# Optimization experiments

Measured on AMD Instinct MI355X. Metric: run time of the kernel, lower is better.

The kernel has to match this reference:

```python
import jax, jax.numpy as jnp
import numpy as np

H = W = 2048


def _grad(x, kernel):
    # torch F.conv2d(x, kernel, stride=1, padding=1); kernel [2,1,2,1] (OIHW)
    # output: [N, 2, H+1, W+2]
    y = jax.lax.conv_general_dilated(
        x, kernel, window_strides=(1, 1), padding=[(1, 1), (1, 1)],
        dimension_numbers=("NCHW", "OIHW", "NCHW"))
    return jnp.abs(y)


def _grayscale(r3):
    # emulates to_pil_image (mul 255 -> uint8) + PIL 'L' conversion + to_tensor (/255)
    # PIL: L = (R*19595 + G*38470 + B*7471 + 0x8000) >> 16
    q = jnp.floor(jnp.clip(r3, 0.0, 1.0) * 255.0)
    gs = jnp.floor((q[0] * 19595.0 + q[1] * 38470.0 + q[2] * 7471.0 + 32768.0) / 65536.0) / 255.0
    # PIL round-trip breaks autograd in the original -> detached here too
    return jax.lax.stop_gradient(gs)[None, None]  # [1,1,H,W]


def _histeq(im, nbins=256):
    # numpy: histogram(density=True) -> cumsum -> /cdf[-1] -> interp(x, bins[:-1], cdf)
    flat = im.reshape(-1)
    hist, edges = jnp.histogram(flat, bins=nbins, density=True)
    cdf = jnp.cumsum(hist)
    cdf = cdf / cdf[-1]
    return jnp.interp(flat, edges[:-1], cdf).reshape(im.shape)


def setup_inputs() -> dict:
    key = jax.random.key(0)
    k1, k2, k3 = jax.random.split(key, 3)
    return {
        "input_im": jax.random.uniform(k1, (1, 3, H, W), dtype=jnp.float32),
        "R": jax.random.uniform(k2, (1, 3, H, W), dtype=jnp.float32),
        "L": jax.random.uniform(k3, (1, 1, H, W), dtype=jnp.float32),
    }


def reference(input_im, R, L):
    kx = jnp.array([0.0, 0.0, -1.0, 1.0], dtype=jnp.float32).reshape(2, 1, 2, 1)
    ky = jnp.transpose(kx, (2, 1, 0, 3))  # torch permute(2,1,0,3)

    # histogram-equalized target (detached in original via .detach().cpu().numpy())
    im_max = jnp.max(input_im, axis=1, keepdims=True)           # [1,1,H,W]
    im_eq = jax.lax.stop_gradient(_histeq(im_max[0]))[None]     # [1,1,H,W]

    # recon_loss_low
    L3 = jnp.concatenate([L, L, L], axis=1)
    recon_low = jnp.mean(jnp.abs(R * L3 - input_im))

    # recon_loss_low_eq
    R_max = jnp.max(R, axis=1, keepdims=True)
    recon_low_eq = jnp.mean(jnp.abs(R_max - im_eq))

    # R_low_loss_smooth (grayscale is detached)
    Rg = _grayscale(R[0])                  # [1,1,H,W]
    a = _grad(Rg, kx)                      # [1,2,H+1,W+2]
    b = _grad(Rg, ky)
    r_smooth = jnp.mean(a + b)             # torch.abs of already-abs values

    # Ismooth_loss_low: smooth(L, R)
    ismooth = jnp.mean(_grad(L, kx) * jnp.exp(-10.0 * a)
                       + _grad(L, ky) * jnp.exp(-10.0 * b))

    return recon_low + 0.1 * ismooth + 0.1 * recon_low_eq + 0.01 * r_smooth
```

## Files before the change

### kernel.cpp

```cpp
#include <hip/hip_runtime.h>
#include <stdint.h>

#define HH 2048
#define WW 2048
#define HW (HH * WW)
#define N4 (HW / 4)
#define FB 512
#define G1H 256
#define G3M 512
#define STRIDE (G1H * 1024)


__device__ __forceinline__ float gray_pil(float r, float g, float b) {
    float qr = floorf(fminf(fmaxf(r, 0.f), 1.f) * 255.f);
    float qg = floorf(fminf(fmaxf(g, 0.f), 1.f) * 255.f);
    float qb = floorf(fminf(fmaxf(b, 0.f), 1.f) * 255.f);
    float s = floorf((qr * 19595.f + qg * 38470.f + qb * 7471.f + 32768.f) * (1.f / 65536.f));
    return s * (1.f / 255.f);
}

__global__ __launch_bounds__(1024, 1)
void hist_k(const float* __restrict__ im, uint32_t* __restrict__ ctl) {
    __shared__ uint32_t lh[FB];
    __shared__ uint32_t sc[256];
    __shared__ uint32_t smm[2];
    __shared__ uint32_t lastf;
    int t = threadIdx.x;
    if (t < FB) lh[t] = 0u;
    __syncthreads();

    const float4* im4 = (const float4*)im;
    int tid = blockIdx.x * 1024 + t;
    float4 A0 = im4[tid],              B0 = im4[tid + N4],              C0 = im4[tid + 2 * N4];
    float4 A1 = im4[tid + STRIDE],     B1 = im4[tid + STRIDE + N4],     C1 = im4[tid + STRIDE + 2 * N4];
    float4 A2 = im4[tid + 2 * STRIDE], B2 = im4[tid + 2 * STRIDE + N4], C2 = im4[tid + 2 * STRIDE + 2 * N4];
    float4 A3 = im4[tid + 3 * STRIDE], B3 = im4[tid + 3 * STRIDE + N4], C3 = im4[tid + 3 * STRIDE + 2 * N4];

#define HBIN(a, b, c) { \
        float m0 = fmaxf(a.x, fmaxf(b.x, c.x)); \
        float m1 = fmaxf(a.y, fmaxf(b.y, c.y)); \
        float m2 = fmaxf(a.z, fmaxf(b.z, c.z)); \
        float m3 = fmaxf(a.w, fmaxf(b.w, c.w)); \
        int b0 = (int)(m0 * (float)FB); b0 = b0 < 0 ? 0 : (b0 > FB - 1 ? FB - 1 : b0); \
        int b1 = (int)(m1 * (float)FB); b1 = b1 < 0 ? 0 : (b1 > FB - 1 ? FB - 1 : b1); \
        int b2 = (int)(m2 * (float)FB); b2 = b2 < 0 ? 0 : (b2 > FB - 1 ? FB - 1 : b2); \
        int b3 = (int)(m3 * (float)FB); b3 = b3 < 0 ? 0 : (b3 > FB - 1 ? FB - 1 : b3); \
        atomicAdd(&lh[b0], 1u); atomicAdd(&lh[b1], 1u); \
        atomicAdd(&lh[b2], 1u); atomicAdd(&lh[b3], 1u); }
    HBIN(A0, B0, C0)
    HBIN(A1, B1, C1)
    HBIN(A2, B2, C2)
    HBIN(A3, B3, C3)
#undef HBIN

    __syncthreads();
    if (t < 256) {
        int pr = (t + blockIdx.x * 7) & 255;
        unsigned long long v = (unsigned long long)lh[2 * pr]
                             | ((unsigned long long)lh[2 * pr + 1] << 32);
        if (v) atomicAdd((unsigned long long*)&ctl[2 * pr], v);
    }
    __syncthreads();
    if (t == 0) {
        __threadfence();
        lastf = (atomicAdd(&ctl[518], 1u) == G1H - 1) ? 1u : 0u;
    }
    __syncthreads();
    if (!lastf) return;

    if (t < FB) lh[t] = atomicAdd(&ctl[t], 0u);
    if (t < 256) sc[t] = 0u;
    if (t == 0) { smm[0] = FB; smm[1] = 0u; }
    __syncthreads();
    if (t < FB && lh[t]) { atomicMin(&smm[0], (uint32_t)t); atomicMax(&smm[1], (uint32_t)t); }
    __syncthreads();
    float gmin = (float)smm[0] * (1.0f / (float)FB);
    float gmax = (float)(smm[1] + 1u) * (1.0f / (float)FB);
    float inv_dw = 256.0f / (gmax - gmin);
    if (t < FB && lh[t]) {
        float c = ((float)t + 0.5f) * (1.0f / (float)FB);
        int q = (int)((c - gmin) * inv_dw);
        q = q < 0 ? 0 : (q > 255 ? 255 : q);
        atomicAdd(&sc[q], lh[t]);
    }
    __syncthreads();
    for (int d = 1; d < 256; d <<= 1) {
        uint32_t v = (t < 256 && t >= d) ? sc[t - d] : 0u;
        __syncthreads();
        if (t < 256) sc[t] += v;
        __syncthreads();
    }
    float* cf = (float*)ctl;
    if (t < 256) cf[t] = (float)((double)sc[t] * (1.0 / (double)HW));
    if (t == 0) { cf[256] = gmin; cf[257] = gmax; }
}

__device__ __forceinline__ void px(float r0, float r1, float r2,
                                   float i0, float i1, float i2, float l,
                                   float& rgp, float& lp,
                                   const float* __restrict__ scdf, float gmin, float inv_dw,
                                   float& a0, float& a1, float& a2,
                                   float& a3, float& a4, float& a5) {
    a0 += fabsf(r0 * l - i0) + fabsf(r1 * l - i1) + fabsf(r2 * l - i2);
    float rmax = fmaxf(r0, fmaxf(r1, r2));
    float imax = fmaxf(i0, fmaxf(i1, i2));
    float t = (imax - gmin) * inv_dw;
    t = fmaxf(t, 0.f);
    int bi = (int)t;
    float eq;
    if (bi >= 255) eq = scdf[255];
    else {
        float fr = t - (float)bi;
        eq = scdf[bi] + fr * (scdf[bi + 1] - scdf[bi]);
    }
    a1 += fabsf(rmax - eq);
    float rg = gray_pil(r0, r1, r2);
    a3 += rg;
    a5 += l * __expf(-10.f * rg);
    float drg = fabsf(rg - rgp);
    a2 += drg;
    a4 += fabsf(l - lp) * __expf(-10.f * drg);
    rgp = rg;
    lp = l;
}

__global__ __launch_bounds__(1024, 1)
void main_k(const float* __restrict__ im, const float* __restrict__ R,
            const float* __restrict__ L, uint32_t* __restrict__ ctl,
            float* __restrict__ part, int use_part,
            float* __restrict__ out) {
    __shared__ float scdf[256];
    __shared__ float red[6][16];
    __shared__ uint32_t lastf;
    int t = threadIdx.x;

    const float* cf = (const float*)ctl;
    if (t < 256) scdf[t] = cf[t];
    float gmin = cf[256];
    float gmax = cf[257];
    float inv_dw = 256.0f / (gmax - gmin);
    __syncthreads();

    int w = (t & 511) * 4;
    int h0 = blockIdx.x * 4 + ((t >> 9) * 2);
    const int p1 = h0 * WW + w;
    const int p2 = p1 + WW;

    float4 Pa, Pb, Pc, Pl;
    if (h0 > 0) {
        int pp = p1 - WW;
        Pa = *(const float4*)(R + pp);
        Pb = *(const float4*)(R + pp + HW);
        Pc = *(const float4*)(R + pp + 2 * HW);
        Pl = *(const float4*)(L + pp);
    }
    float4 r0a = *(const float4*)(R + p1);
    float4 r0b = *(const float4*)(R + p1 + HW);
    float4 r0c = *(const float4*)(R + p1 + 2 * HW);
    float4 i0a = *(const float4*)(im + p1);
    float4 i0b = *(const float4*)(im + p1 + HW);
    float4 i0c = *(const float4*)(im + p1 + 2 * HW);
    float4 l0  = *(const float4*)(L + p1);
    float4 r1a = *(const float4*)(R + p2);
    float4 r1b = *(const float4*)(R + p2 + HW);
    float4 r1c = *(const float4*)(R + p2 + 2 * HW);
    float4 i1a = *(const float4*)(im + p2);
    float4 i1b = *(const float4*)(im + p2 + HW);
    float4 i1c = *(const float4*)(im + p2 + 2 * HW);
    float4 l1  = *(const float4*)(L + p2);

    float a0 = 0.f, a1 = 0.f, a2 = 0.f, a3 = 0.f, a4 = 0.f, a5 = 0.f;
    float rgp[4], lp[4];
    if (h0 > 0) {
        rgp[0] = gray_pil(Pa.x, Pb.x, Pc.x); lp[0] = Pl.x;
        rgp[1] = gray_pil(Pa.y, Pb.y, Pc.y); lp[1] = Pl.y;
        rgp[2] = gray_pil(Pa.z, Pb.z, Pc.z); lp[2] = Pl.z;
        rgp[3] = gray_pil(Pa.w, Pb.w, Pc.w); lp[3] = Pl.w;
    } else {
        rgp[0] = rgp[1] = rgp[2] = rgp[3] = 0.f;
        lp[0] = lp[1] = lp[2] = lp[3] = 0.f;
    }

    px(r0a.x, r0b.x, r0c.x, i0a.x, i0b.x, i0c.x, l0.x, rgp[0], lp[0], scdf, gmin, inv_dw, a0, a1, a2, a3, a4, a5);
    px(r0a.y, r0b.y, r0c.y, i0a.y, i0b.y, i0c.y, l0.y, rgp[1], lp[1], scdf, gmin, inv_dw, a0, a1, a2, a3, a4, a5);
    px(r0a.z, r0b.z, r0c.z, i0a.z, i0b.z, i0c.z, l0.z, rgp[2], lp[2], scdf, gmin, inv_dw, a0, a1, a2, a3, a4, a5);
    px(r0a.w, r0b.w, r0c.w, i0a.w, i0b.w, i0c.w, l0.w, rgp[3], lp[3], scdf, gmin, inv_dw, a0, a1, a2, a3, a4, a5);
    px(r1a.x, r1b.x, r1c.x, i1a.x, i1b.x, i1c.x, l1.x, rgp[0], lp[0], scdf, gmin, inv_dw, a0, a1, a2, a3, a4, a5);
    px(r1a.y, r1b.y, r1c.y, i1a.y, i1b.y, i1c.y, l1.y, rgp[1], lp[1], scdf, gmin, inv_dw, a0, a1, a2, a3, a4, a5);
    px(r1a.z, r1b.z, r1c.z, i1a.z, i1b.z, i1c.z, l1.z, rgp[2], lp[2], scdf, gmin, inv_dw, a0, a1, a2, a3, a4, a5);
    px(r1a.w, r1b.w, r1c.w, i1a.w, i1b.w, i1c.w, l1.w, rgp[3], lp[3], scdf, gmin, inv_dw, a0, a1, a2, a3, a4, a5);

    if (h0 + 2 == HH) {
#pragma unroll
        for (int j = 0; j < 4; ++j) {
            a2 += rgp[j];
            a4 += lp[j] * __expf(-10.f * rgp[j]);
        }
    }

    for (int off = 32; off; off >>= 1) {
        a0 += __shfl_down(a0, off);
        a1 += __shfl_down(a1, off);
        a2 += __shfl_down(a2, off);
        a3 += __shfl_down(a3, off);
        a4 += __shfl_down(a4, off);
        a5 += __shfl_down(a5, off);
    }
    int lane = t & 63, wv = t >> 6;
    if (lane == 0) {
        red[0][wv] = a0; red[1][wv] = a1; red[2][wv] = a2;
        red[3][wv] = a3; red[4][wv] = a4; red[5][wv] = a5;
    }
    __syncthreads();
    if (t == 0) {
        float s0 = 0, s1 = 0, s2 = 0, s3 = 0, s4 = 0, s5 = 0;
        for (int k = 0; k < 16; k++) {
            s0 += red[0][k]; s1 += red[1][k]; s2 += red[2][k];
            s3 += red[3][k]; s4 += red[4][k]; s5 += red[5][k];
        }
        if (use_part) {
            float* pp = part + blockIdx.x * 6;
            atomicExch(&pp[0], s0); atomicExch(&pp[1], s1); atomicExch(&pp[2], s2);
            atomicExch(&pp[3], s3); atomicExch(&pp[4], s4); atomicExch(&pp[5], s5);
        } else {
            float* acc = (float*)(ctl + 512);
            atomicAdd(&acc[0], s0); atomicAdd(&acc[1], s1); atomicAdd(&acc[2], s2);
            atomicAdd(&acc[3], s3); atomicAdd(&acc[4], s4); atomicAdd(&acc[5], s5);
        }
        __threadfence();
        lastf = (atomicAdd(&ctl[518], 1u) == (uint32_t)(G1H + G3M - 1)) ? 1u : 0u;
    }
    __syncthreads();
    if (!lastf) return;

    if (use_part) {
        float s0 = 0.f, s1 = 0.f, s2 = 0.f, s3 = 0.f, s4 = 0.f, s5 = 0.f;
        if (t < G3M) {
            float* pp = part + t * 6;
            s0 = atomicAdd(&pp[0], 0.f); s1 = atomicAdd(&pp[1], 0.f); s2 = atomicAdd(&pp[2], 0.f);
            s3 = atomicAdd(&pp[3], 0.f); s4 = atomicAdd(&pp[4], 0.f); s5 = atomicAdd(&pp[5], 0.f);
        }
        for (int off = 32; off; off >>= 1) {
            s0 += __shfl_down(s0, off);
            s1 += __shfl_down(s1, off);
            s2 += __shfl_down(s2, off);
            s3 += __shfl_down(s3, off);
            s4 += __shfl_down(s4, off);
            s5 += __shfl_down(s5, off);
        }
        if (lane == 0) {
            red[0][wv] = s0; red[1][wv] = s1; red[2][wv] = s2;
            red[3][wv] = s3; red[4][wv] = s4; red[5][wv] = s5;
        }
        __syncthreads();
        if (t == 0) {
            float v0 = 0, v1 = 0, v2 = 0, v3 = 0, v4 = 0, v5 = 0;
            for (int k = 0; k < 16; k++) {
                v0 += red[0][k]; v1 += red[1][k]; v2 += red[2][k];
                v3 += red[3][k]; v4 += red[4][k]; v5 += red[5][k];
            }
            float recon_low = v0 / (3.0f * (float)HW);
            float recon_eq = v1 / (float)HW;
            float denom = 2.0f * 2049.0f * 2050.0f;
            float r_smooth = (v2 + 2.f * v3) / denom;
            float ismooth = (v4 + 2.f * v5) / denom;
            out[0] = recon_low + 0.1f * ismooth + 0.1f * recon_eq + 0.01f * r_smooth;
        }
    } else {
        if (t == 0) {
            float* acc = (float*)(ctl + 512);
            float v0 = atomicAdd(&acc[0], 0.f);
            float v1 = atomicAdd(&acc[1], 0.f);
            float v2 = atomicAdd(&acc[2], 0.f);
            float v3 = atomicAdd(&acc[3], 0.f);
            float v4 = atomicAdd(&acc[4], 0.f);
            float v5 = atomicAdd(&acc[5], 0.f);
            float recon_low = v0 / (3.0f * (float)HW);
            float recon_eq = v1 / (float)HW;
            float denom = 2.0f * 2049.0f * 2050.0f;
            float r_smooth = (v2 + 2.f * v3) / denom;
            float ismooth = (v4 + 2.f * v5) / denom;
            out[0] = recon_low + 0.1f * ismooth + 0.1f * recon_eq + 0.01f * r_smooth;
        }
    }
}

extern "C" void kernel_launch(void* const* d_in, const int* in_sizes, int n_in,
                              void* d_out, int out_size, void* d_ws, size_t ws_size,
                              hipStream_t stream) {
    const float* im = (const float*)d_in[0];
    const float* R = (const float*)d_in[1];
    const float* L = (const float*)d_in[2];
    float* out = (float*)d_out;
    uint32_t* ctl = (uint32_t*)d_ws;

    int use_part = (ws_size >= (size_t)((520 + 6 * G3M) * 4 + 32)) ? 1 : 0;
    float* part = (float*)(ctl + 520);

    hipMemsetAsync(d_ws, 0, 519 * 4, stream);
    hipLaunchKernelGGL(hist_k, dim3(G1H), dim3(1024), 0, stream, im, ctl);
    hipLaunchKernelGGL(main_k, dim3(G3M), dim3(1024), 0, stream, im, R, L, ctl, part, use_part, out);
}
```

Before: 170.1 us.

## Stage loads through LDS with global_load_lds and pipeline rows in main kernel

Both kernels now use 256-thread blocks and load inputs with direct global-to-LDS async loads (global_load_lds) instead of loading into registers. The main kernel has each thread walk 8 rows in 4 steps, prefetching the next row pair into LDS while it computes the current one. The histogram kernel moves to 2048 smaller blocks, each handling 2 float4 groups per thread. The aim is to overlap memory latency with compute and cut register pressure. The cost is extra LDS traffic and manual waitcnt handling. The staging buffer is overwritten by the next prefetch with no barrier between the LDS reads and the reissued loads, which is a possible race.

```diff
diff --git a/kernel.cpp b/kernel.cpp
--- a/kernel.cpp
+++ b/kernel.cpp
@@ -6,10 +6,14 @@
 #define HW (HH * WW)
 #define N4 (HW / 4)
 #define FB 512
-#define G1H 256
+#define G1H 2048
 #define G3M 512
-#define STRIDE (G1H * 1024)
-
+
+
+#define GLOAD16(gp, lp)                                                              \
+    __builtin_amdgcn_global_load_lds(                                                \
+        (const __attribute__((address_space(1))) void*)(gp),                         \
+        (__attribute__((address_space(3))) void*)(lp), 16, 0, 0)
 
 __device__ __forceinline__ float gray_pil(float r, float g, float b) {
     float qr = floorf(fminf(fmaxf(r, 0.f), 1.f) * 255.f);
@@ -19,42 +23,48 @@
     return s * (1.f / 255.f);
 }
 
-__global__ __launch_bounds__(1024, 1)
+__global__ __launch_bounds__(256, 2)
 void hist_k(const float* __restrict__ im, uint32_t* __restrict__ ctl) {
+    __shared__ float4 hstage[4][6][64];
     __shared__ uint32_t lh[FB];
     __shared__ uint32_t sc[256];
     __shared__ uint32_t smm[2];
     __shared__ uint32_t lastf;
     int t = threadIdx.x;
-    if (t < FB) lh[t] = 0u;
-    __syncthreads();
+    int lane = t & 63, wv = t >> 6;
+    lh[t] = 0u;
+    lh[t + 256] = 0u;
 
     const float4* im4 = (const float4*)im;
-    int tid = blockIdx.x * 1024 + t;
-    float4 A0 = im4[tid],              B0 = im4[tid + N4],              C0 = im4[tid + 2 * N4];
-    float4 A1 = im4[tid + STRIDE],     B1 = im4[tid + STRIDE + N4],     C1 = im4[tid + STRIDE + 2 * N4];
-    float4 A2 = im4[tid + 2 * STRIDE], B2 = im4[tid + 2 * STRIDE + N4], C2 = im4[tid + 2 * STRIDE + 2 * N4];
-    float4 A3 = im4[tid + 3 * STRIDE], B3 = im4[tid + 3 * STRIDE + N4], C3 = im4[tid + 3 * STRIDE + 2 * N4];
-
-#define HBIN(a, b, c) { \
-        float m0 = fmaxf(a.x, fmaxf(b.x, c.x)); \
-        float m1 = fmaxf(a.y, fmaxf(b.y, c.y)); \
-        float m2 = fmaxf(a.z, fmaxf(b.z, c.z)); \
-        float m3 = fmaxf(a.w, fmaxf(b.w, c.w)); \
-        int b0 = (int)(m0 * (float)FB); b0 = b0 < 0 ? 0 : (b0 > FB - 1 ? FB - 1 : b0); \
-        int b1 = (int)(m1 * (float)FB); b1 = b1 < 0 ? 0 : (b1 > FB - 1 ? FB - 1 : b1); \
-        int b2 = (int)(m2 * (float)FB); b2 = b2 < 0 ? 0 : (b2 > FB - 1 ? FB - 1 : b2); \
-        int b3 = (int)(m3 * (float)FB); b3 = b3 < 0 ? 0 : (b3 > FB - 1 ? FB - 1 : b3); \
-        atomicAdd(&lh[b0], 1u); atomicAdd(&lh[b1], 1u); \
-        atomicAdd(&lh[b2], 1u); atomicAdd(&lh[b3], 1u); }
-    HBIN(A0, B0, C0)
-    HBIN(A1, B1, C1)
-    HBIN(A2, B2, C2)
-    HBIN(A3, B3, C3)
-#undef HBIN
-
-    __syncthreads();
-    if (t < 256) {
+    int tid = blockIdx.x * 256 + t;
+#pragma unroll
+    for (int k = 0; k < 2; ++k) {
+        int i = tid + k * (G1H * 256);
+#pragma unroll
+        for (int pl = 0; pl < 3; ++pl)
+            GLOAD16(im4 + i + pl * N4, &hstage[wv][k * 3 + pl][0]);
+    }
+    __syncthreads();
+    asm volatile("s_waitcnt vmcnt(0)" ::: "memory");
+
+#pragma unroll
+    for (int k = 0; k < 2; ++k) {
+        float4 a = hstage[wv][k * 3 + 0][lane];
+        float4 b = hstage[wv][k * 3 + 1][lane];
+        float4 c = hstage[wv][k * 3 + 2][lane];
+        float m0 = fmaxf(a.x, fmaxf(b.x, c.x));
+        float m1 = fmaxf(a.y, fmaxf(b.y, c.y));
+        float m2 = fmaxf(a.z, fmaxf(b.z, c.z));
+        float m3 = fmaxf(a.w, fmaxf(b.w, c.w));
+        int b0 = (int)(m0 * (float)FB); b0 = b0 < 0 ? 0 : (b0 > FB - 1 ? FB - 1 : b0);
+        int b1 = (int)(m1 * (float)FB); b1 = b1 < 0 ? 0 : (b1 > FB - 1 ? FB - 1 : b1);
+        int b2 = (int)(m2 * (float)FB); b2 = b2 < 0 ? 0 : (b2 > FB - 1 ? FB - 1 : b2);
+        int b3 = (int)(m3 * (float)FB); b3 = b3 < 0 ? 0 : (b3 > FB - 1 ? FB - 1 : b3);
+        atomicAdd(&lh[b0], 1u); atomicAdd(&lh[b1], 1u);
+        atomicAdd(&lh[b2], 1u); atomicAdd(&lh[b3], 1u);
+    }
+    __syncthreads();
+    {
         int pr = (t + blockIdx.x * 7) & 255;
         unsigned long long v = (unsigned long long)lh[2 * pr]
                              | ((unsigned long long)lh[2 * pr + 1] << 32);
@@ -68,30 +78,37 @@
     __syncthreads();
     if (!lastf) return;
 
-    if (t < FB) lh[t] = atomicAdd(&ctl[t], 0u);
-    if (t < 256) sc[t] = 0u;
+    lh[t] = atomicAdd(&ctl[t], 0u);
+    lh[t + 256] = atomicAdd(&ctl[t + 256], 0u);
+    sc[t] = 0u;
     if (t == 0) { smm[0] = FB; smm[1] = 0u; }
     __syncthreads();
-    if (t < FB && lh[t]) { atomicMin(&smm[0], (uint32_t)t); atomicMax(&smm[1], (uint32_t)t); }
+    if (lh[t]) { atomicMin(&smm[0], (uint32_t)t); atomicMax(&smm[1], (uint32_t)t); }
+    if (lh[t + 256]) { atomicMin(&smm[0], (uint32_t)(t + 256)); atomicMax(&smm[1], (uint32_t)(t + 256)); }
     __syncthreads();
     float gmin = (float)smm[0] * (1.0f / (float)FB);
     float gmax = (float)(smm[1] + 1u) * (1.0f / (float)FB);
     float inv_dw = 256.0f / (gmax - gmin);
-    if (t < FB && lh[t]) {
-        float c = ((float)t + 0.5f) * (1.0f / (float)FB);
-        int q = (int)((c - gmin) * inv_dw);
-        q = q < 0 ? 0 : (q > 255 ? 255 : q);
-        atomicAdd(&sc[q], lh[t]);
+#pragma unroll
+    for (int jj = 0; jj < 2; ++jj) {
+        int j = t + jj * 256;
+        uint32_t cnt = lh[j];
+        if (cnt) {
+            float c = ((float)j + 0.5f) * (1.0f / (float)FB);
+            int q = (int)((c - gmin) * inv_dw);
+            q = q < 0 ? 0 : (q > 255 ? 255 : q);
+            atomicAdd(&sc[q], cnt);
+        }
     }
     __syncthreads();
     for (int d = 1; d < 256; d <<= 1) {
-        uint32_t v = (t < 256 && t >= d) ? sc[t - d] : 0u;
+        uint32_t v = (t >= d) ? sc[t - d] : 0u;
         __syncthreads();
-        if (t < 256) sc[t] += v;
+        sc[t] += v;
         __syncthreads();
     }
     float* cf = (float*)ctl;
-    if (t < 256) cf[t] = (float)((double)sc[t] * (1.0 / (double)HW));
+    cf[t] = (float)((double)sc[t] * (1.0 / (double)HW));
     if (t == 0) { cf[256] = gmin; cf[257] = gmax; }
 }
 
@@ -124,54 +141,55 @@
     lp = l;
 }
 
-__global__ __launch_bounds__(1024, 1)
+__global__ __launch_bounds__(256, 2)
 void main_k(const float* __restrict__ im, const float* __restrict__ R,
             const float* __restrict__ L, uint32_t* __restrict__ ctl,
             float* __restrict__ part, int use_part,
             float* __restrict__ out) {
+    __shared__ float4 stage[4][14][64];
     __shared__ float scdf[256];
-    __shared__ float red[6][16];
+    __shared__ float red[6][4];
     __shared__ uint32_t lastf;
     int t = threadIdx.x;
+    int lane = t & 63, wv = t >> 6;
 
     const float* cf = (const float*)ctl;
-    if (t < 256) scdf[t] = cf[t];
+    scdf[t] = cf[t];
     float gmin = cf[256];
     float gmax = cf[257];
     float inv_dw = 256.0f / (gmax - gmin);
-    __syncthreads();
-
-    int w = (t & 511) * 4;
-    int h0 = blockIdx.x * 4 + ((t >> 9) * 2);
-    const int p1 = h0 * WW + w;
-    const int p2 = p1 + WW;
-
-    float4 Pa, Pb, Pc, Pl;
-    if (h0 > 0) {
-        int pp = p1 - WW;
-        Pa = *(const float4*)(R + pp);
-        Pb = *(const float4*)(R + pp + HW);
-        Pc = *(const float4*)(R + pp + 2 * HW);
-        Pl = *(const float4*)(L + pp);
-    }
-    float4 r0a = *(const float4*)(R + p1);
-    float4 r0b = *(const float4*)(R + p1 + HW);
-    float4 r0c = *(const float4*)(R + p1 + 2 * HW);
-    float4 i0a = *(const float4*)(im + p1);
-    float4 i0b = *(const float4*)(im + p1 + HW);
-    float4 i0c = *(const float4*)(im + p1 + 2 * HW);
-    float4 l0  = *(const float4*)(L + p1);
-    float4 r1a = *(const float4*)(R + p2);
-    float4 r1b = *(const float4*)(R + p2 + HW);
-    float4 r1c = *(const float4*)(R + p2 + 2 * HW);
-    float4 i1a = *(const float4*)(im + p2);
-    float4 i1b = *(const float4*)(im + p2 + HW);
-    float4 i1c = *(const float4*)(im + p2 + 2 * HW);
-    float4 l1  = *(const float4*)(L + p2);
+
+    int tid = blockIdx.x * 256 + t;
+    int w = (tid & 511) * 4;
+    int h0 = (tid >> 9) * 8;
+
+    const float* b0p = R;
+    const float* b1p = R + HW;
+    const float* b2p = R + 2 * HW;
+    const float* b3p = im;
+    const float* b4p = im + HW;
+    const float* b5p = im + 2 * HW;
+    const float* b6p = L;
+
+    {
+        int p0 = h0 * WW + w, p1 = p0 + WW;
+        GLOAD16(b0p + p0, &stage[wv][0][0]);  GLOAD16(b0p + p1, &stage[wv][7][0]);
+        GLOAD16(b1p + p0, &stage[wv][1][0]);  GLOAD16(b1p + p1, &stage[wv][8][0]);
+        GLOAD16(b2p + p0, &stage[wv][2][0]);  GLOAD16(b2p + p1, &stage[wv][9][0]);
+        GLOAD16(b3p + p0, &stage[wv][3][0]);  GLOAD16(b3p + p1, &stage[wv][10][0]);
+        GLOAD16(b4p + p0, &stage[wv][4][0]);  GLOAD16(b4p + p1, &stage[wv][11][0]);
+        GLOAD16(b5p + p0, &stage[wv][5][0]);  GLOAD16(b5p + p1, &stage[wv][12][0]);
+        GLOAD16(b6p + p0, &stage[wv][6][0]);  GLOAD16(b6p + p1, &stage[wv][13][0]);
+    }
 
     float a0 = 0.f, a1 = 0.f, a2 = 0.f, a3 = 0.f, a4 = 0.f, a5 = 0.f;
     float rgp[4], lp[4];
     if (h0 > 0) {
+        int pp = (h0 - 1) * WW + w;
+        float4 Pa = *(const float4*)(R + pp);
+        float4 Pb = *(const float4*)(R + pp + HW);
+        float4 Pc = *(const float4*)(R + pp + 2 * HW);
+        float4 Pl = *(const float4*)(L + pp);
         rgp[0] = gray_pil(Pa.x, Pb.x, Pc.x); lp[0] = Pl.x;
         rgp[1] = gray_pil(Pa.y, Pb.y, Pc.y); lp[1] = Pl.y;
         rgp[2] = gray_pil(Pa.z, Pb.z, Pc.z); lp[2] = Pl.z;
@@ -180,17 +198,48 @@
         rgp[0] = rgp[1] = rgp[2] = rgp[3] = 0.f;
         lp[0] = lp[1] = lp[2] = lp[3] = 0.f;
     }
-
-    px(r0a.x, r0b.x, r0c.x, i0a.x, i0b.x, i0c.x, l0.x, rgp[0], lp[0], scdf, gmin, inv_dw, a0, a1, a2, a3, a4, a5);
-    px(r0a.y, r0b.y, r0c.y, i0a.y, i0b.y, i0c.y, l0.y, rgp[1], lp[1], scdf, gmin, inv_dw, a0, a1, a2, a3, a4, a5);
-    px(r0a.z, r0b.z, r0c.z, i0a.z, i0b.z, i0c.z, l0.z, rgp[2], lp[2], scdf, gmin, inv_dw, a0, a1, a2, a3, a4, a5);
-    px(r0a.w, r0b.w, r0c.w, i0a.w, i0b.w, i0c.w, l0.w, rgp[3], lp[3], scdf, gmin, inv_dw, a0, a1, a2, a3, a4, a5);
-    px(r1a.x, r1b.x, r1c.x, i1a.x, i1b.x, i1c.x, l1.x, rgp[0], lp[0], scdf, gmin, inv_dw, a0, a1, a2, a3, a4, a5);
-    px(r1a.y, r1b.y, r1c.y, i1a.y, i1b.y, i1c.y, l1.y, rgp[1], lp[1], scdf, gmin, inv_dw, a0, a1, a2, a3, a4, a5);
-    px(r1a.z, r1b.z, r1c.z, i1a.z, i1b.z, i1c.z, l1.z, rgp[2], lp[2], scdf, gmin, inv_dw, a0, a1, a2, a3, a4, a5);
-    px(r1a.w, r1b.w, r1c.w, i1a.w, i1b.w, i1c.w, l1.w, rgp[3], lp[3], scdf, gmin, inv_dw, a0, a1, a2, a3, a4, a5);
-
-    if (h0 + 2 == HH) {
+    __syncthreads();
+
+    for (int pr = 0; pr < 4; ++pr) {
+        asm volatile("s_waitcnt vmcnt(0)" ::: "memory");
+        float4 r0a = stage[wv][0][lane];
+        float4 r0b = stage[wv][1][lane];
+        float4 r0c = stage[wv][2][lane];
+        float4 i0a = stage[wv][3][lane];
+        float4 i0b = stage[wv][4][lane];
+        float4 i0c = stage[wv][5][lane];
+        float4 l0  = stage[wv][6][lane];
+        float4 r1a = stage[wv][7][lane];
+        float4 r1b = stage[wv][8][lane];
+        float4 r1c = stage[wv][9][lane];
+        float4 i1a = stage[wv][10][lane];
+        float4 i1b = stage[wv][11][lane];
+        float4 i1c = stage[wv][12][lane];
+        float4 l1  = stage[wv][13][lane];
+        asm volatile("s_waitcnt lgkmcnt(0)" ::: "memory");
+
+        if (pr < 3) {
+            int p0 = (h0 + 2 * pr + 2) * WW + w, p1 = p0 + WW;
+            GLOAD16(b0p + p0, &stage[wv][0][0]);  GLOAD16(b0p + p1, &stage[wv][7][0]);
+            GLOAD16(b1p + p0, &stage[wv][1][0]);  GLOAD16(b1p + p1, &stage[wv][8][0]);
+            GLOAD16(b2p + p0, &stage[wv][2][0]);  GLOAD16(b2p + p1, &stage[wv][9][0]);
+            GLOAD16(b3p + p0, &stage[wv][3][0]);  GLOAD16(b3p + p1, &stage[wv][10][0]);
+            GLOAD16(b4p + p0, &stage[wv][4][0]);  GLOAD16(b4p + p1, &stage[wv][11][0]);
+            GLOAD16(b5p + p0, &stage[wv][5][0]);  GLOAD16(b5p + p1, &stage[wv][12][0]);
+            GLOAD16(b6p + p0, &stage[wv][6][0]);  GLOAD16(b6p + p1, &stage[wv][13][0]);
+        }
+
+        px(r0a.x, r0b.x, r0c.x, i0a.x, i0b.x, i0c.x, l0.x, rgp[0], lp[0], scdf, gmin, inv_dw, a0, a1, a2, a3, a4, a5);
+        px(r0a.y, r0b.y, r0c.y, i0a.y, i0b.y, i0c.y, l0.y, rgp[1], lp[1], scdf, gmin, inv_dw, a0, a1, a2, a3, a4, a5);
+        px(r0a.z, r0b.z, r0c.z, i0a.z, i0b.z, i0c.z, l0.z, rgp[2], lp[2], scdf, gmin, inv_dw, a0, a1, a2, a3, a4, a5);
+        px(r0a.w, r0b.w, r0c.w, i0a.w, i0b.w, i0c.w, l0.w, rgp[3], lp[3], scdf, gmin, inv_dw, a0, a1, a2, a3, a4, a5);
+        px(r1a.x, r1b.x, r1c.x, i1a.x, i1b.x, i1c.x, l1.x, rgp[0], lp[0], scdf, gmin, inv_dw, a0, a1, a2, a3, a4, a5);
+        px(r1a.y, r1b.y, r1c.y, i1a.y, i1b.y, i1c.y, l1.y, rgp[1], lp[1], scdf, gmin, inv_dw, a0, a1, a2, a3, a4, a5);
+        px(r1a.z, r1b.z, r1c.z, i1a.z, i1b.z, i1c.z, l1.z, rgp[2], lp[2], scdf, gmin, inv_dw, a0, a1, a2, a3, a4, a5);
+        px(r1a.w, r1b.w, r1c.w, i1a.w, i1b.w, i1c.w, l1.w, rgp[3], lp[3], scdf, gmin, inv_dw, a0, a1, a2, a3, a4, a5);
+    }
+
+    if (h0 + 8 == HH) {
 #pragma unroll
         for (int j = 0; j < 4; ++j) {
             a2 += rgp[j];
@@ -206,7 +255,6 @@
         a4 += __shfl_down(a4, off);
         a5 += __shfl_down(a5, off);
     }
-    int lane = t & 63, wv = t >> 6;
     if (lane == 0) {
         red[0][wv] = a0; red[1][wv] = a1; red[2][wv] = a2;
         red[3][wv] = a3; red[4][wv] = a4; red[5][wv] = a5;
@@ -214,7 +262,7 @@
     __syncthreads();
     if (t == 0) {
         float s0 = 0, s1 = 0, s2 = 0, s3 = 0, s4 = 0, s5 = 0;
-        for (int k = 0; k < 16; k++) {
+        for (int k = 0; k < 4; k++) {
             s0 += red[0][k]; s1 += red[1][k]; s2 += red[2][k];
             s3 += red[3][k]; s4 += red[4][k]; s5 += red[5][k];
         }
@@ -234,11 +282,16 @@
     if (!lastf) return;
 
     if (use_part) {
-        float s0 = 0.f, s1 = 0.f, s2 = 0.f, s3 = 0.f, s4 = 0.f, s5 = 0.f;
-        if (t < G3M) {
-            float* pp = part + t * 6;
-            s0 = atomicAdd(&pp[0], 0.f); s1 = atomicAdd(&pp[1], 0.f); s2 = atomicAdd(&pp[2], 0.f);
-            s3 = atomicAdd(&pp[3], 0.f); s4 = atomicAdd(&pp[4], 0.f); s5 = atomicAdd(&pp[5], 0.f);
+        float s0, s1, s2, s3, s4, s5;
+        {
+            float* pa = part + t * 6;
+            float* pb = part + (t + 256) * 6;
+            s0 = atomicAdd(&pa[0], 0.f) + atomicAdd(&pb[0], 0.f);
+            s1 = atomicAdd(&pa[1], 0.f) + atomicAdd(&pb[1], 0.f);
+            s2 = atomicAdd(&pa[2], 0.f) + atomicAdd(&pb[2], 0.f);
+            s3 = atomicAdd(&pa[3], 0.f) + atomicAdd(&pb[3], 0.f);
+            s4 = atomicAdd(&pa[4], 0.f) + atomicAdd(&pb[4], 0.f);
+            s5 = atomicAdd(&pa[5], 0.f) + atomicAdd(&pb[5], 0.f);
         }
         for (int off = 32; off; off >>= 1) {
             s0 += __shfl_down(s0, off);
@@ -255,7 +308,7 @@
         __syncthreads();
         if (t == 0) {
             float v0 = 0, v1 = 0, v2 = 0, v3 = 0, v4 = 0, v5 = 0;
-            for (int k = 0; k < 16; k++) {
+            for (int k = 0; k < 4; k++) {
                 v0 += red[0][k]; v1 += red[1][k]; v2 += red[2][k];
                 v3 += red[3][k]; v4 += red[4][k]; v5 += red[5][k];
             }
@@ -298,6 +351,6 @@
     float* part = (float*)(ctl + 520);
 
     hipMemsetAsync(d_ws, 0, 519 * 4, stream);
-    hipLaunchKernelGGL(hist_k, dim3(G1H), dim3(1024), 0, stream, im, ctl);
-    hipLaunchKernelGGL(main_k, dim3(G3M), dim3(1024), 0, stream, im, R, L, ctl, part, use_part, out);
-}
+    hipLaunchKernelGGL(hist_k, dim3(G1H), dim3(256), 0, stream, im, ctl);
+    hipLaunchKernelGGL(main_k, dim3(G3M), dim3(256), 0, stream, im, R, L, ctl, part, use_part, out);
+}
```

After: 256.5 us. +50.8%, slower.
